# Kernel optimization log

Measured on AMD Instinct MI355X. Metric: run time of the kernel, lower is better.

## Reference

```python
import jax, jax.numpy as jnp
import numpy as np

C = 256
CI = C // 2  # inter_channel = 128
B, H, W = 8, 64, 64


def setup_inputs() -> dict:
    key = jax.random.key(0)
    ks = jax.random.split(key, 9)
    s = 0.02
    return {
        "x": jax.random.normal(ks[0], (B, C, H, W), jnp.float32),
        "w_phi": jax.random.normal(ks[1], (CI, C), jnp.float32) * s,
        "b_phi": jax.random.normal(ks[2], (CI,), jnp.float32) * s,
        "w_theta": jax.random.normal(ks[3], (CI, C), jnp.float32) * s,
        "b_theta": jax.random.normal(ks[4], (CI,), jnp.float32) * s,
        "w_g": jax.random.normal(ks[5], (CI, C), jnp.float32) * s,
        "b_g": jax.random.normal(ks[6], (CI,), jnp.float32) * s,
        "w_mask": jax.random.normal(ks[7], (C, CI), jnp.float32) * s,
        "b_mask": jax.random.normal(ks[8], (C,), jnp.float32) * s,
    }


def reference(x, w_phi, b_phi, w_theta, b_theta, w_g, b_g, w_mask, b_mask):
    b, c, h, w = x.shape
    n = h * w
    xf = x.reshape(b, c, n)  # [b, c, n]
    # 1x1 convs == per-position channel projections
    phi = jnp.einsum('dc,bcn->bdn', w_phi, xf) + b_phi[:, None]      # [b, ci, n]
    theta = jnp.einsum('dc,bcn->bnd', w_theta, xf) + b_theta[None, None, :]  # [b, n, ci]
    g = jnp.einsum('dc,bcn->bnd', w_g, xf) + b_g[None, None, :]      # [b, n, ci]
    # full self-attention over spatial positions (no scaling, as in source)
    scores = jnp.einsum('bnd,bdm->bnm', theta, phi)                  # [b, n, n]
    attn = jax.nn.softmax(scores, axis=-1)
    y = jnp.einsum('bnm,bmd->bnd', attn, g)                          # [b, n, ci]
    # mask conv (1x1) back to channel dim + residual
    mask = jnp.einsum('cd,bnd->bcn', w_mask, y) + b_mask[:, None]    # [b, c, n]
    return mask.reshape(b, c, h, w) + x
```

## Files before the change

kernel.cpp:

```cpp
#include <hip/hip_runtime.h>

#define BB 8
#define CC 256
#define DD 128
#define NN 4096

#define LOG2E 1.44269504f
#define MSHIFT 32.0f

typedef __attribute__((ext_vector_type(8))) short short8;
typedef __attribute__((ext_vector_type(4))) short short4v;
typedef __attribute__((ext_vector_type(4))) float f32x4;
typedef __attribute__((ext_vector_type(16))) float f32x16;
typedef __attribute__((ext_vector_type(4))) unsigned int u32x4;

static __device__ __forceinline__ unsigned short f2bf(float f) {
    unsigned u = __builtin_bit_cast(unsigned, f);
    u += 0x7FFFu + ((u >> 16) & 1u);
    return (unsigned short)(u >> 16);
}
static __device__ __forceinline__ float bf2f(unsigned short h) {
    unsigned u = ((unsigned)h) << 16;
    return __builtin_bit_cast(float, u);
}
static __device__ __forceinline__ short8 pack8(float4 a, float4 b) {
    short8 r;
    r[0] = (short)f2bf(a.x); r[1] = (short)f2bf(a.y);
    r[2] = (short)f2bf(a.z); r[3] = (short)f2bf(a.w);
    r[4] = (short)f2bf(b.x); r[5] = (short)f2bf(b.y);
    r[6] = (short)f2bf(b.z); r[7] = (short)f2bf(b.w);
    return r;
}
static __device__ __forceinline__ unsigned cvtpk_bf16(float lo, float hi) {
    unsigned r;
    asm("v_cvt_pk_bf16_f32 %0, %1, %2" : "=v"(r) : "v"(lo), "v"(hi));
    return r;
}
static __device__ __forceinline__ void pl32swap(unsigned &a, unsigned &b) {
#if __has_builtin(__builtin_amdgcn_permlane32_swap)
    auto r = __builtin_amdgcn_permlane32_swap((int)a, (int)b, false, false);
    a = (unsigned)r[0]; b = (unsigned)r[1];
#else
    asm("v_permlane32_swap_b32 %0, %1" : "+v"(a), "+v"(b));
#endif
}
static __device__ __forceinline__ void gll16(const void* g, void* l) {
    __builtin_amdgcn_global_load_lds(
        (const __attribute__((address_space(1))) unsigned int*)g,
        (__attribute__((address_space(3))) unsigned int*)l, 16, 0, 0);
}
#define VMWAIT(N) asm volatile("s_waitcnt vmcnt(" #N ")" ::: "memory")

__global__ __launch_bounds__(512, 2) void k_proj(
        const float* __restrict__ x,
        const float* __restrict__ w_phi, const float* __restrict__ b_phi,
        const float* __restrict__ w_theta, const float* __restrict__ b_theta,
        const float* __restrict__ w_g, const float* __restrict__ b_g,
        unsigned short* __restrict__ qws, unsigned short* __restrict__ kws,
        unsigned short* __restrict__ vtws) {
    __shared__ __align__(16) unsigned short xs[128][72];
    __shared__ __align__(16) unsigned short rp[128][136];
    int nb = blockIdx.x * 128, b = blockIdx.y;
    int t = threadIdx.x, lane = t & 63, wave = t >> 6;
    int l16 = lane & 15, l4 = lane >> 4;
    int wd = wave & 3, wn = wave >> 2;

    f32x4 a_th[2][4], a_ph[2][4], a_g[2][4];
#pragma unroll
    for (int mf = 0; mf < 2; mf++)
#pragma unroll
        for (int nf = 0; nf < 4; nf++)
#pragma unroll
            for (int e = 0; e < 4; e++) { a_th[mf][nf][e] = 0.f; a_ph[mf][nf][e] = 0.f; a_g[mf][nf][e] = 0.f; }

    const float* xpb = x + (size_t)b * CC * NN;

    for (int kc = 0; kc < 4; kc++) {
        int c0k = kc * 64;
        __syncthreads();
        {
            float4 xv[4];
#pragma unroll
            for (int j = 0; j < 4; j++) {
                int idx = t + 512 * j;
                int cr = idx >> 5, pos = idx & 31;
                xv[j] = *(const float4*)(xpb + (size_t)(c0k + cr) * NN + nb + pos * 4);
            }
#pragma unroll
            for (int j = 0; j < 4; j++) {
                int idx = t + 512 * j;
                int cr = idx >> 5, pos = idx & 31;
                int col = (cr + 8 * (pos >> 2)) & 63;
                xs[pos * 4 + 0][col] = f2bf(xv[j].x);
                xs[pos * 4 + 1][col] = f2bf(xv[j].y);
                xs[pos * 4 + 2][col] = f2bf(xv[j].z);
                xs[pos * 4 + 3][col] = f2bf(xv[j].w);
            }
        }
        __syncthreads();
        short8 af_t[2][2], af_p[2][2], af_g[2][2];
#pragma unroll
        for (int mf = 0; mf < 2; mf++)
#pragma unroll
            for (int ic = 0; ic < 2; ic++) {
                int d = wd * 32 + mf * 16 + l16;
                int co = c0k + ic * 32 + l4 * 8;
                const float* wpt = w_theta + d * CC + co;
                const float* wpp = w_phi   + d * CC + co;
                const float* wpg = w_g     + d * CC + co;
                af_t[mf][ic] = pack8(*(const float4*)wpt, *(const float4*)(wpt + 4));
                af_p[mf][ic] = pack8(*(const float4*)wpp, *(const float4*)(wpp + 4));
                af_g[mf][ic] = pack8(*(const float4*)wpg, *(const float4*)(wpg + 4));
            }
#pragma unroll
        for (int nf = 0; nf < 4; nf++)
#pragma unroll
            for (int ic = 0; ic < 2; ic++) {
                int ncol = (ic * 32 + l4 * 8 + 8 * (wn * 4 + nf)) & 63;
                short8 bfr = *(const short8*)&xs[wn * 64 + nf * 16 + l16][ncol];
                a_th[0][nf] = __builtin_amdgcn_mfma_f32_16x16x32_bf16(af_t[0][ic], bfr, a_th[0][nf], 0, 0, 0);
                a_th[1][nf] = __builtin_amdgcn_mfma_f32_16x16x32_bf16(af_t[1][ic], bfr, a_th[1][nf], 0, 0, 0);
                a_ph[0][nf] = __builtin_amdgcn_mfma_f32_16x16x32_bf16(af_p[0][ic], bfr, a_ph[0][nf], 0, 0, 0);
                a_ph[1][nf] = __builtin_amdgcn_mfma_f32_16x16x32_bf16(af_p[1][ic], bfr, a_ph[1][nf], 0, 0, 0);
                a_g[0][nf]  = __builtin_amdgcn_mfma_f32_16x16x32_bf16(af_g[0][ic], bfr, a_g[0][nf], 0, 0, 0);
                a_g[1][nf]  = __builtin_amdgcn_mfma_f32_16x16x32_bf16(af_g[1][ic], bfr, a_g[1][nf], 0, 0, 0);
            }
    }
    __syncthreads();

#pragma unroll
    for (int mf = 0; mf < 2; mf++) {
        int d0 = wd * 32 + mf * 16 + l4 * 4;
        float bb[4];
#pragma unroll
        for (int r = 0; r < 4; r++) bb[r] = b_theta[d0 + r];
#pragma unroll
        for (int nf = 0; nf < 4; nf++) {
            short4v pk;
#pragma unroll
            for (int r = 0; r < 4; r++) pk[r] = (short)f2bf((a_th[mf][nf][r] + bb[r]) * LOG2E);
            *(short4v*)&rp[wn * 64 + nf * 16 + l16][d0] = pk;
        }
    }
    __syncthreads();
    {
        unsigned short* outp = qws + (size_t)b * NN * DD;
#pragma unroll
        for (int i = 0; i < 4; i++) {
            int idx = t + 512 * i;
            int n = idx >> 4, dd = (idx & 15) * 8;
            *(short8*)(outp + (size_t)(nb + n) * DD + dd) = *(const short8*)&rp[n][dd];
        }
    }
    __syncthreads();

#pragma unroll
    for (int mf = 0; mf < 2; mf++) {
        int d0 = wd * 32 + mf * 16 + l4 * 4;
        float bb[4];
#pragma unroll
        for (int r = 0; r < 4; r++) bb[r] = b_phi[d0 + r];
#pragma unroll
        for (int nf = 0; nf < 4; nf++) {
            short4v pk;
#pragma unroll
            for (int r = 0; r < 4; r++) pk[r] = (short)f2bf(a_ph[mf][nf][r] + bb[r]);
            *(short4v*)&rp[wn * 64 + nf * 16 + l16][d0] = pk;
        }
    }
    __syncthreads();
    {
        unsigned short* outp = kws + (size_t)b * NN * DD;
#pragma unroll
        for (int i = 0; i < 4; i++) {
            int idx = t + 512 * i;
            int n = idx >> 4, dd = (idx & 15) * 8;
            *(short8*)(outp + (size_t)(nb + n) * DD + dd) = *(const short8*)&rp[n][dd];
        }
    }
    __syncthreads();

#pragma unroll
    for (int mf = 0; mf < 2; mf++) {
        int drow = wd * 32 + mf * 16 + l4 * 4;
        float bb[4];
#pragma unroll
        for (int r = 0; r < 4; r++) bb[r] = b_g[drow + r];
#pragma unroll
        for (int nf = 0; nf < 4; nf++)
#pragma unroll
            for (int r = 0; r < 4; r++)
                rp[drow + r][wn * 64 + nf * 16 + l16] = f2bf(a_g[mf][nf][r] + bb[r]);
    }
    __syncthreads();
    {
        unsigned short* outp = vtws + (size_t)b * DD * NN;
#pragma unroll
        for (int i = 0; i < 4; i++) {
            int idx = t + 512 * i;
            int d = idx >> 4, n0s = (idx & 15) * 8;
            *(short8*)(outp + (size_t)d * NN + nb + n0s) = *(const short8*)&rp[d][n0s];
        }
    }
}

__global__ __launch_bounds__(256, 2) void k_flash(
        const unsigned short* __restrict__ q, const unsigned short* __restrict__ kk,
        const unsigned short* __restrict__ vt, unsigned short* __restrict__ opart,
        float* __restrict__ lsums) {
    __shared__ __align__(16) unsigned char smem[65536];

    int bid = blockIdx.x;
    int b   = bid & 7;
    int rem = bid >> 3;
    int ks  = rem >> 5;
    int qt  = rem & 31;
    int qb  = qt * 128;

    int t = threadIdx.x, lane = t & 63, wave = t >> 6;
    int l31 = lane & 31, hi = lane >> 5;

    const unsigned short* qp = q  + (size_t)b * NN * DD;
    const unsigned short* kp = kk + (size_t)b * NN * DD;
    const unsigned short* vp = vt + (size_t)b * DD * NN;

    short8 qreg[8];
    {
        int qrow = qb + wave * 32 + l31;
#pragma unroll
        for (int kc = 0; kc < 8; kc++)
            qreg[kc] = *(const short8*)(qp + (size_t)qrow * DD + kc * 16 + hi * 8);
    }

    int koff[2], voff[2];
#pragma unroll
    for (int j = 0; j < 2; j++) {
        int seg = wave * 2 + j;
        int krow = seg * 4 + (lane >> 4);
        koff[j] = krow * DD + (((lane & 15) ^ (krow & 7)) << 3);
        int vrow = seg * 16 + (lane >> 2);
        voff[j] = vrow * NN + (((lane & 3) ^ ((vrow ^ (vrow >> 2)) & 3)) << 3);
    }

    int kvo[8], vvo[2];
    {
        int e = l31 & 7;
#pragma unroll
        for (int kc = 0; kc < 8; kc++)
            kvo[kc] = l31 * 256 + ((((kc << 1) | hi) ^ e) << 4);
        int sw = (l31 ^ (l31 >> 2)) & 3;
#pragma unroll
        for (int c = 0; c < 2; c++)
            vvo[c] = l31 * 64 + ((((c << 1) | hi) ^ sw) << 4);
    }

    f32x16 o[4];
#pragma unroll
    for (int df = 0; df < 4; df++)
#pragma unroll
        for (int e = 0; e < 16; e++) o[df][e] = 0.f;
    float lsum0 = 0.f, lsum1 = 0.f;

    int kbase = ks * (NN / 2);
    const int NIT = (NN / 2) / 32;

#pragma unroll
    for (int pt = 0; pt < 2; pt++) {
        int mb = kbase + pt * 32;
        char* Kb = (char*)smem + pt * 16384;
#pragma unroll
        for (int j = 0; j < 2; j++) {
            int seg = wave * 2 + j;
            gll16(kp + (size_t)mb * DD + koff[j], Kb + seg * 1024);
            gll16(vp + mb + voff[j], Kb + 8192 + seg * 1024);
        }
    }

#pragma unroll 4
    for (int it = 0; it < NIT; ++it) {
        char* Kb = (char*)smem + (it & 3) * 16384;
        char* Vb = Kb + 8192;

        if (it + 2 < NIT) {
            int mb2 = kbase + (it + 2) * 32;
            char* KbW = (char*)smem + ((it + 2) & 3) * 16384;
#pragma unroll
            for (int j = 0; j < 2; j++) {
                int seg = wave * 2 + j;
                gll16(kp + (size_t)mb2 * DD + koff[j], KbW + seg * 1024);
                gll16(vp + mb2 + voff[j], KbW + 8192 + seg * 1024);
            }
            VMWAIT(8);
        } else if (it + 1 < NIT) {
            VMWAIT(4);
        } else {
            VMWAIT(0);
        }
        __builtin_amdgcn_s_barrier();
        asm volatile("" ::: "memory");

        f32x16 s;
#pragma unroll
        for (int e = 0; e < 16; e++) s[e] = -MSHIFT;
        __builtin_amdgcn_s_setprio(1);
#pragma unroll
        for (int kc = 0; kc < 8; kc++) {
            short8 a0 = *(const short8*)(Kb + kvo[kc]);
            s = __builtin_amdgcn_mfma_f32_32x32x16_bf16(a0, qreg[kc], s, 0, 0, 0);
        }
        __builtin_amdgcn_s_setprio(0);

        u32x4 pa[2];
        {
            float p[16];
#pragma unroll
            for (int r = 0; r < 16; r++) {
                p[r] = __builtin_exp2f(s[r]);
                if (r & 1) lsum1 += p[r]; else lsum0 += p[r];
            }
#pragma unroll
            for (int h = 0; h < 2; h++) {
                unsigned a0 = cvtpk_bf16(p[8 * h + 0], p[8 * h + 1]);
                unsigned a1 = cvtpk_bf16(p[8 * h + 2], p[8 * h + 3]);
                unsigned b0 = cvtpk_bf16(p[8 * h + 4], p[8 * h + 5]);
                unsigned b1 = cvtpk_bf16(p[8 * h + 6], p[8 * h + 7]);
                pl32swap(a0, b0);
                pl32swap(a1, b1);
                u32x4 v; v[0] = a0; v[1] = a1; v[2] = b0; v[3] = b1;
                pa[h] = v;
            }
        }

        __builtin_amdgcn_s_setprio(1);
#pragma unroll
        for (int df = 0; df < 4; df++) {
#pragma unroll
            for (int c = 0; c < 2; c++) {
                short8 vb = *(const short8*)(Vb + df * 2048 + vvo[c]);
                o[df] = __builtin_amdgcn_mfma_f32_32x32x16_bf16(
                    __builtin_bit_cast(short8, pa[c]), vb, o[df], 0, 0, 0);
            }
        }
        __builtin_amdgcn_s_setprio(0);
    }

    {
        float lsum = lsum0 + lsum1;
        float tot = lsum + __shfl_xor(lsum, 32);
        if (lane < 32)
            lsums[((size_t)ks * BB + b) * NN + qb + wave * 32 + l31] = tot;
    }
    __syncthreads();
    unsigned short (*Ox)[136] = (unsigned short (*)[136])smem;
#pragma unroll
    for (int df = 0; df < 4; df++)
#pragma unroll
        for (int r = 0; r < 16; r++) {
            int qr = (r & 3) + 8 * (r >> 2) + 4 * hi;
            Ox[wave * 32 + qr][df * 32 + l31] = f2bf(o[df][r]);
        }
    __syncthreads();
    unsigned short* op = opart + (((size_t)ks * BB + b) * NN + qb) * DD;
#pragma unroll
    for (int i = 0; i < 8; i++) {
        int idx = t + 256 * i;
        int nr = idx >> 4, c0 = (idx & 15) * 8;
        *(short8*)(op + (size_t)nr * DD + c0) = *(const short8*)&Ox[nr][c0];
    }
}

__global__ __launch_bounds__(256) void k_maskout(
        const unsigned short* __restrict__ opart, const float* __restrict__ lsums,
        const float* __restrict__ w_mask, const float* __restrict__ b_mask,
        const float* __restrict__ x, float* __restrict__ out) {
    __shared__ __align__(16) unsigned char pool[52480];
    unsigned short (*Ys)[136] = (unsigned short (*)[136])pool;
    float (*Os)[68] = (float (*)[68])(pool + 17408);
    float* invl = (float*)(pool + 52224);
    int nb = blockIdx.x * 64, b = blockIdx.y;
    int t = threadIdx.x, lane = t & 63, wave = t >> 6;
    int l16 = lane & 15, l4 = lane >> 4;

    const unsigned short* o0 = opart + ((size_t)b * NN + nb) * DD;
    const unsigned short* o1 = opart + (((size_t)BB + b) * NN + nb) * DD;
    if (t < 64) {
        float ls0 = lsums[(size_t)b * NN + nb + t];
        float ls1 = lsums[((size_t)BB + b) * NN + nb + t];
        invl[t] = 1.0f / (ls0 + ls1);
    }
    __syncthreads();
#pragma unroll
    for (int i = 0; i < 4; i++) {
        int idx = t + 256 * i;
        int nr = idx >> 4, d0 = (idx & 15) * 8;
        short8 a = *(const short8*)(o0 + (size_t)nr * DD + d0);
        short8 c = *(const short8*)(o1 + (size_t)nr * DD + d0);
        float inv = invl[nr];
        short8 yv;
#pragma unroll
        for (int j = 0; j < 8; j++)
            yv[j] = (short)f2bf((bf2f((unsigned short)a[j]) + bf2f((unsigned short)c[j])) * inv);
        *(short8*)&Ys[nr][d0] = yv;
    }
    __syncthreads();

    for (int cs = 0; cs < 2; cs++) {
        f32x4 acc[2][4];
#pragma unroll
        for (int mf = 0; mf < 2; mf++)
#pragma unroll
            for (int nf = 0; nf < 4; nf++)
#pragma unroll
                for (int e = 0; e < 4; e++) acc[mf][nf][e] = 0.f;

#pragma unroll
        for (int kc = 0; kc < 4; kc++) {
            int d0 = kc * 32 + l4 * 8;
            short8 af[2];
#pragma unroll
            for (int mf = 0; mf < 2; mf++) {
                int c = cs * 128 + wave * 32 + mf * 16 + l16;
                const float* wp = w_mask + c * DD + d0;
                af[mf] = pack8(*(const float4*)wp, *(const float4*)(wp + 4));
            }
#pragma unroll
            for (int nf = 0; nf < 4; nf++) {
                short8 bfr = *(const short8*)&Ys[nf * 16 + l16][d0];
#pragma unroll
                for (int mf = 0; mf < 2; mf++)
                    acc[mf][nf] = __builtin_amdgcn_mfma_f32_16x16x32_bf16(af[mf], bfr, acc[mf][nf], 0, 0, 0);
            }
        }
        __syncthreads();

#pragma unroll
        for (int mf = 0; mf < 2; mf++) {
            int c0 = wave * 32 + mf * 16 + l4 * 4;
            float bb[4];
#pragma unroll
            for (int r = 0; r < 4; r++) bb[r] = b_mask[cs * 128 + c0 + r];
#pragma unroll
            for (int r = 0; r < 4; r++)
#pragma unroll
                for (int nf = 0; nf < 4; nf++)
                    Os[c0 + r][nf * 16 + l16] = acc[mf][nf][r] + bb[r];
        }
        __syncthreads();

        const float* xp = x + (size_t)b * CC * NN + (size_t)cs * 128 * NN + nb;
        float* op = out + (size_t)b * CC * NN + (size_t)cs * 128 * NN + nb;
#pragma unroll
        for (int i = 0; i < 8; i++) {
            int idx = t + 256 * i;
            int c = idx >> 4, nq = (idx & 15) * 4;
            float4 osv = *(const float4*)&Os[c][nq];
            float4 xv = *(const float4*)(xp + (size_t)c * NN + nq);
            float4 ov;
            ov.x = osv.x + xv.x; ov.y = osv.y + xv.y;
            ov.z = osv.z + xv.z; ov.w = osv.w + xv.w;
            *(float4*)(op + (size_t)c * NN + nq) = ov;
        }
    }
}

extern "C" void kernel_launch(void* const* d_in, const int* in_sizes, int n_in,
                              void* d_out, int out_size, void* d_ws, size_t ws_size,
                              hipStream_t stream) {
    const float* x       = (const float*)d_in[0];
    const float* w_phi   = (const float*)d_in[1];
    const float* b_phi   = (const float*)d_in[2];
    const float* w_theta = (const float*)d_in[3];
    const float* b_theta = (const float*)d_in[4];
    const float* w_g     = (const float*)d_in[5];
    const float* b_g     = (const float*)d_in[6];
    const float* w_mask  = (const float*)d_in[7];
    const float* b_mask  = (const float*)d_in[8];
    float* out = (float*)d_out;

    char* ws = (char*)d_ws;
    unsigned short* opart = (unsigned short*)(ws);
    unsigned short* qw    = (unsigned short*)(ws + ((size_t)16 << 20));
    unsigned short* kw    = (unsigned short*)(ws + ((size_t)24 << 20));
    unsigned short* vtw   = (unsigned short*)(ws + ((size_t)32 << 20));
    float*          lsums = (float*)(ws + ((size_t)40 << 20));

    k_proj<<<dim3(NN / 128, BB), 512, 0, stream>>>(x, w_phi, b_phi, w_theta, b_theta,
                                                   w_g, b_g, qw, kw, vtw);
    k_flash<<<dim3(512, 1, 1), 256, 0, stream>>>(qw, kw, vtw, opart, lsums);
    k_maskout<<<dim3(NN / 64, BB), 256, 0, stream>>>(opart, lsums, w_mask, b_mask, x, out);
}
```

Measured before the change: 220.6 us.

## Software-pipeline flash loop: overlap next-tile QK MFMAs with current-tile exp

The attention inner loop is restructured so the QK^T MFMAs for key tile it+1 are interleaved with the exp2/accumulate/bf16-pack work for tile it. A prologue computes the first score tile, and the loop is manually unrolled by two with ping-pong score registers. The prefetch wait is relaxed so only the next K tile must be resident. The aim is to hide transcendental and VALU latency behind matrix-core work, at the cost of extra live registers and one redundant QK computation on the final iteration.

```diff
diff --git a/kernel.cpp b/kernel.cpp
--- a/kernel.cpp
+++ b/kernel.cpp
@@ -204,6 +204,78 @@
     }
 }
 
+#define QKSTEP(SN, KBN, KC) \
+    SN = __builtin_amdgcn_mfma_f32_32x32x16_bf16( \
+        *(const short8*)((KBN) + kvo[KC]), qreg[KC], SN, 0, 0, 0);
+
+#define PABUILD(PA, Pa, Pb, Pc, Pd, Pe, Pf_, Pg, Ph) {                                \
+    unsigned x0 = cvtpk_bf16(Pa, Pb);                                                 \
+    unsigned x1 = cvtpk_bf16(Pc, Pd);                                                 \
+    unsigned y0 = cvtpk_bf16(Pe, Pf_);                                                \
+    unsigned y1 = cvtpk_bf16(Pg, Ph);                                                 \
+    pl32swap(x0, y0); pl32swap(x1, y1);                                               \
+    PA[0] = x0; PA[1] = x1; PA[2] = y0; PA[3] = y1; }
+
+#define FBODY(IT, SC, SN) {                                                           \
+    if ((IT) + 2 < NIT) {                                                             \
+        int mb2 = kbase + ((IT) + 2) * 32;                                            \
+        char* W = (char*)smem + (((IT) + 2) & 3) * 16384;                             \
+        gll16(kp + (size_t)mb2 * DD + koff[0], W + (wave * 2 + 0) * 1024);            \
+        gll16(kp + (size_t)mb2 * DD + koff[1], W + (wave * 2 + 1) * 1024);            \
+        gll16(vp + mb2 + voff[0], W + 8192 + (wave * 2 + 0) * 1024);                  \
+        gll16(vp + mb2 + voff[1], W + 8192 + (wave * 2 + 1) * 1024);                  \
+        VMWAIT(4);                                                                    \
+    } else {                                                                          \
+        VMWAIT(0);                                                                    \
+    }                                                                                 \
+    __builtin_amdgcn_s_barrier();                                                     \
+    asm volatile("" ::: "memory");                                                    \
+    char* KbN = (char*)smem + (((IT) + 1) & 3) * 16384;                               \
+    char* Vb  = (char*)smem + ((IT) & 3) * 16384 + 8192;                              \
+    _Pragma("unroll") for (int e = 0; e < 16; e++) SN[e] = -MSHIFT;                   \
+    float p0, p1, p2, p3, p4, p5, p6, p7, p8, p9, p10, p11, p12, p13, p14, p15;       \
+    __builtin_amdgcn_s_setprio(1);                                                    \
+    p0 = __builtin_exp2f(SC[0]);  lsum0 += p0;                                        \
+    p1 = __builtin_exp2f(SC[1]);  lsum1 += p1;                                        \
+    p2 = __builtin_exp2f(SC[2]);  lsum0 += p2;                                        \
+    p3 = __builtin_exp2f(SC[3]);  lsum1 += p3;                                        \
+    QKSTEP(SN, KbN, 0) QKSTEP(SN, KbN, 1)                                             \
+    p4 = __builtin_exp2f(SC[4]);  lsum0 += p4;                                        \
+    p5 = __builtin_exp2f(SC[5]);  lsum1 += p5;                                        \
+    p6 = __builtin_exp2f(SC[6]);  lsum0 += p6;                                        \
+    p7 = __builtin_exp2f(SC[7]);  lsum1 += p7;                                        \
+    QKSTEP(SN, KbN, 2) QKSTEP(SN, KbN, 3)                                             \
+    u32x4 paA; PABUILD(paA, p0, p1, p2, p3, p4, p5, p6, p7)                           \
+    p8  = __builtin_exp2f(SC[8]);  lsum0 += p8;                                       \
+    p9  = __builtin_exp2f(SC[9]);  lsum1 += p9;                                       \
+    p10 = __builtin_exp2f(SC[10]); lsum0 += p10;                                      \
+    p11 = __builtin_exp2f(SC[11]); lsum1 += p11;                                      \
+    QKSTEP(SN, KbN, 4) QKSTEP(SN, KbN, 5)                                             \
+    p12 = __builtin_exp2f(SC[12]); lsum0 += p12;                                      \
+    p13 = __builtin_exp2f(SC[13]); lsum1 += p13;                                      \
+    p14 = __builtin_exp2f(SC[14]); lsum0 += p14;                                      \
+    p15 = __builtin_exp2f(SC[15]); lsum1 += p15;                                      \
+    QKSTEP(SN, KbN, 6) QKSTEP(SN, KbN, 7)                                             \
+    u32x4 paB; PABUILD(paB, p8, p9, p10, p11, p12, p13, p14, p15)                     \
+    o[0] = __builtin_amdgcn_mfma_f32_32x32x16_bf16(                                   \
+        __builtin_bit_cast(short8, paA), *(const short8*)(Vb + 0 * 2048 + vvo[0]), o[0], 0, 0, 0); \
+    o[1] = __builtin_amdgcn_mfma_f32_32x32x16_bf16(                                   \
+        __builtin_bit_cast(short8, paA), *(const short8*)(Vb + 1 * 2048 + vvo[0]), o[1], 0, 0, 0); \
+    o[2] = __builtin_amdgcn_mfma_f32_32x32x16_bf16(                                   \
+        __builtin_bit_cast(short8, paA), *(const short8*)(Vb + 2 * 2048 + vvo[0]), o[2], 0, 0, 0); \
+    o[3] = __builtin_amdgcn_mfma_f32_32x32x16_bf16(                                   \
+        __builtin_bit_cast(short8, paA), *(const short8*)(Vb + 3 * 2048 + vvo[0]), o[3], 0, 0, 0); \
+    o[0] = __builtin_amdgcn_mfma_f32_32x32x16_bf16(                                   \
+        __builtin_bit_cast(short8, paB), *(const short8*)(Vb + 0 * 2048 + vvo[1]), o[0], 0, 0, 0); \
+    o[1] = __builtin_amdgcn_mfma_f32_32x32x16_bf16(                                   \
+        __builtin_bit_cast(short8, paB), *(const short8*)(Vb + 1 * 2048 + vvo[1]), o[1], 0, 0, 0); \
+    o[2] = __builtin_amdgcn_mfma_f32_32x32x16_bf16(                                   \
+        __builtin_bit_cast(short8, paB), *(const short8*)(Vb + 2 * 2048 + vvo[1]), o[2], 0, 0, 0); \
+    o[3] = __builtin_amdgcn_mfma_f32_32x32x16_bf16(                                   \
+        __builtin_bit_cast(short8, paB), *(const short8*)(Vb + 3 * 2048 + vvo[1]), o[3], 0, 0, 0); \
+    __builtin_amdgcn_s_setprio(0);                                                    \
+}
+
 __global__ __launch_bounds__(256, 2) void k_flash(
         const unsigned short* __restrict__ q, const unsigned short* __restrict__ kk,
         const unsigned short* __restrict__ vt, unsigned short* __restrict__ opart,
@@ -275,73 +347,24 @@
             gll16(vp + mb + voff[j], Kb + 8192 + seg * 1024);
         }
     }
-
-#pragma unroll 4
-    for (int it = 0; it < NIT; ++it) {
-        char* Kb = (char*)smem + (it & 3) * 16384;
-        char* Vb = Kb + 8192;
-
-        if (it + 2 < NIT) {
-            int mb2 = kbase + (it + 2) * 32;
-            char* KbW = (char*)smem + ((it + 2) & 3) * 16384;
-#pragma unroll
-            for (int j = 0; j < 2; j++) {
-                int seg = wave * 2 + j;
-                gll16(kp + (size_t)mb2 * DD + koff[j], KbW + seg * 1024);
-                gll16(vp + mb2 + voff[j], KbW + 8192 + seg * 1024);
-            }
-            VMWAIT(8);
-        } else if (it + 1 < NIT) {
-            VMWAIT(4);
-        } else {
-            VMWAIT(0);
-        }
-        __builtin_amdgcn_s_barrier();
-        asm volatile("" ::: "memory");
-
-        f32x16 s;
-#pragma unroll
-        for (int e = 0; e < 16; e++) s[e] = -MSHIFT;
+    VMWAIT(4);
+    __builtin_amdgcn_s_barrier();
+    asm volatile("" ::: "memory");
+
+    f32x16 s0, s1;
+#pragma unroll
+    for (int e = 0; e < 16; e++) s0[e] = -MSHIFT;
+    {
+        char* Kb0 = (char*)smem;
         __builtin_amdgcn_s_setprio(1);
-#pragma unroll
-        for (int kc = 0; kc < 8; kc++) {
-            short8 a0 = *(const short8*)(Kb + kvo[kc]);
-            s = __builtin_amdgcn_mfma_f32_32x32x16_bf16(a0, qreg[kc], s, 0, 0, 0);
-        }
+        QKSTEP(s0, Kb0, 0) QKSTEP(s0, Kb0, 1) QKSTEP(s0, Kb0, 2) QKSTEP(s0, Kb0, 3)
+        QKSTEP(s0, Kb0, 4) QKSTEP(s0, Kb0, 5) QKSTEP(s0, Kb0, 6) QKSTEP(s0, Kb0, 7)
         __builtin_amdgcn_s_setprio(0);
-
-        u32x4 pa[2];
-        {
-            float p[16];
-#pragma unroll
-            for (int r = 0; r < 16; r++) {
-                p[r] = __builtin_exp2f(s[r]);
-                if (r & 1) lsum1 += p[r]; else lsum0 += p[r];
-            }
-#pragma unroll
-            for (int h = 0; h < 2; h++) {
-                unsigned a0 = cvtpk_bf16(p[8 * h + 0], p[8 * h + 1]);
-                unsigned a1 = cvtpk_bf16(p[8 * h + 2], p[8 * h + 3]);
-                unsigned b0 = cvtpk_bf16(p[8 * h + 4], p[8 * h + 5]);
-                unsigned b1 = cvtpk_bf16(p[8 * h + 6], p[8 * h + 7]);
-                pl32swap(a0, b0);
-                pl32swap(a1, b1);
-                u32x4 v; v[0] = a0; v[1] = a1; v[2] = b0; v[3] = b1;
-                pa[h] = v;
-            }
-        }
-
-        __builtin_amdgcn_s_setprio(1);
-#pragma unroll
-        for (int df = 0; df < 4; df++) {
-#pragma unroll
-            for (int c = 0; c < 2; c++) {
-                short8 vb = *(const short8*)(Vb + df * 2048 + vvo[c]);
-                o[df] = __builtin_amdgcn_mfma_f32_32x32x16_bf16(
-                    __builtin_bit_cast(short8, pa[c]), vb, o[df], 0, 0, 0);
-            }
-        }
-        __builtin_amdgcn_s_setprio(0);
+    }
+
+    for (int it = 0; it < NIT; it += 2) {
+        FBODY(it, s0, s1)
+        FBODY(it + 1, s1, s0)
     }
 
     {
```

After: 222.7 us. Within noise of the previous version (+1.0%).
